# Kernel tuning notes

Hardware: AMD Instinct MI355X
Metric: run time of the kernel (lower is better)

The kernel has to match this reference:

```python
import jax, jax.numpy as jnp
import numpy as np

N, E, H, L, G, MAX_Z = 100000, 1600000, 128, 3, 1024, 1000
BN_EPS = 1e-5

def setup_inputs() -> dict:
    key = jax.random.key(0)
    ks = jax.random.split(key, 16)
    z = jax.random.randint(ks[0], (N,), 0, MAX_Z)
    edge_index = jax.random.randint(ks[1], (2, E), 0, N)
    batch = jnp.sort(jax.random.randint(ks[2], (N,), 0, G))
    s = 1.0 / np.sqrt(H)
    z_table = jax.random.normal(ks[3], (MAX_Z, H), jnp.float32)
    conv_W1 = jax.random.normal(ks[4], (L, H, H), jnp.float32) * s
    conv_b1 = jnp.zeros((L, H), jnp.float32)
    conv_W2 = jax.random.normal(ks[5], (L, H, H), jnp.float32) * s
    conv_b2 = jnp.zeros((L, H), jnp.float32)
    bn_gamma = jnp.ones((L, H), jnp.float32)
    bn_beta = jnp.zeros((L, H), jnp.float32)
    lin1_W = jax.random.normal(ks[6], (L * H, H), jnp.float32) / np.sqrt(L * H)
    lin1_b = jnp.zeros((H,), jnp.float32)
    lin2_W = jax.random.normal(ks[7], (H, 1), jnp.float32) * s
    lin2_b = jnp.zeros((1,), jnp.float32)
    return {"z": z, "edge_index": edge_index, "batch": batch,
            "z_table": z_table, "conv_W1": conv_W1, "conv_b1": conv_b1,
            "conv_W2": conv_W2, "conv_b2": conv_b2, "bn_gamma": bn_gamma,
            "bn_beta": bn_beta, "lin1_W": lin1_W, "lin1_b": lin1_b,
            "lin2_W": lin2_W, "lin2_b": lin2_b}

def _gin_layer(x, src, dst, W1, b1, W2, b2, gamma, beta):
    # GIN sum aggregation: (1+eps)*x_i + sum_{j->i} x_j  (eps=0)
    agg = x + jax.ops.segment_sum(x[src], dst, num_segments=N)
    h = jax.nn.relu(agg @ W1 + b1)
    h = jax.nn.relu(h @ W2 + b2)
    # BatchNorm1d (training-mode batch statistics over nodes)
    mu = jnp.mean(h, axis=0)
    var = jnp.mean(jnp.square(h - mu), axis=0)
    return gamma * (h - mu) * jax.lax.rsqrt(var + BN_EPS) + beta

def reference(z, edge_index, batch, z_table, conv_W1, conv_b1, conv_W2,
              conv_b2, bn_gamma, bn_beta, lin1_W, lin1_b, lin2_W, lin2_b):
    src, dst = edge_index[0], edge_index[1]
    x = z_table[z]                      # [N, H]
    xs = []
    for l in range(L):
        x = _gin_layer(x, src, dst, conv_W1[l], conv_b1[l], conv_W2[l],
                       conv_b2[l], bn_gamma[l], bn_beta[l])
        xs.append(x)
    feat = jnp.concatenate(xs, axis=1)  # [N, L*H] (jk=True)
    sums = jax.ops.segment_sum(feat, batch, num_segments=G)
    cnt = jax.ops.segment_sum(jnp.ones((N,), feat.dtype), batch, num_segments=G)
    pooled = sums / jnp.maximum(cnt, 1.0)[:, None]   # global_mean_pool [G, L*H]
    h = jax.nn.relu(pooled @ lin1_W + lin1_b)
    # dropout inactive (eval mode)
    return h @ lin2_W + lin2_b          # [G, 1]
```

## Files before the change

### kernel.cpp

```cpp
#include <hip/hip_runtime.h>

#define NN 100000
#define NE 1600000
#define HD 128
#define NL 3
#define NG 1024
#define BN_EPS 1e-5f
#define SCAN_CHUNK 1024

static inline int cdiv(int a, int b) { return (a + b - 1) / b; }

__global__ __launch_bounds__(256) void zero_counts_kernel(int* __restrict__ cnt) {
  int t = blockIdx.x * 256 + threadIdx.x;
  if (t < NN) cnt[t] = 0;
}

__global__ __launch_bounds__(256) void hist_kernel(const int* __restrict__ dstI,
    int* __restrict__ cnt) {
  int e = blockIdx.x * 256 + threadIdx.x;
  if (e < NE) atomicAdd(&cnt[dstI[e]], 1);
}

__global__ __launch_bounds__(256) void scan_block_kernel(const int* __restrict__ cnt,
    int* __restrict__ rowptr, int* __restrict__ bsums) {
  __shared__ int sh[SCAN_CHUNK];
  __shared__ int ts[256];
  int base = blockIdx.x * SCAN_CHUNK;
  for (int i = threadIdx.x; i < SCAN_CHUNK; i += 256)
    sh[i] = (base + i < NN) ? cnt[base + i] : 0;
  __syncthreads();
  int t4 = threadIdx.x * 4;
  int a0 = sh[t4], a1 = sh[t4 + 1], a2 = sh[t4 + 2], a3 = sh[t4 + 3];
  int tsum = a0 + a1 + a2 + a3;
  ts[threadIdx.x] = tsum;
  __syncthreads();
  for (int off = 1; off < 256; off <<= 1) {
    int v = ts[threadIdx.x];
    int u = (threadIdx.x >= off) ? ts[threadIdx.x - off] : 0;
    __syncthreads();
    ts[threadIdx.x] = v + u;
    __syncthreads();
  }
  int texcl = ts[threadIdx.x] - tsum;
  sh[t4] = texcl;
  sh[t4 + 1] = texcl + a0;
  sh[t4 + 2] = texcl + a0 + a1;
  sh[t4 + 3] = texcl + a0 + a1 + a2;
  __syncthreads();
  for (int i = threadIdx.x; i < SCAN_CHUNK; i += 256) {
    int g = base + i;
    if (g < NN) rowptr[g] = sh[i];
  }
  if (threadIdx.x == 255) bsums[blockIdx.x] = ts[255];
}

__global__ void scan_bsums_kernel(int* __restrict__ bsums, int nb) {
  if (threadIdx.x == 0) {
    int run = 0;
    for (int i = 0; i < nb; ++i) { int v = bsums[i]; bsums[i] = run; run += v; }
  }
}

__global__ __launch_bounds__(256) void scan_add_kernel(int* __restrict__ rowptr,
    const int* __restrict__ bsums, int* __restrict__ fill_off) {
  int t = blockIdx.x * 256 + threadIdx.x;
  if (t < NN) {
    int v = rowptr[t] + bsums[t / SCAN_CHUNK];
    rowptr[t] = v;
    fill_off[t] = v;
  }
  if (t == 0) rowptr[NN] = NE;
}

__global__ __launch_bounds__(256) void fill_kernel(const int* __restrict__ srcI,
    const int* __restrict__ dstI, const int* __restrict__ z,
    int* __restrict__ fill_off, int* __restrict__ esrc, int* __restrict__ esrcz) {
  int e = blockIdx.x * 256 + threadIdx.x;
  if (e >= NE) return;
  int s = srcI[e];
  int d = dstI[e];
  int pos = atomicAdd(&fill_off[d], 1);
  esrc[pos] = s;
  esrcz[pos] = z[s];
}

__global__ __launch_bounds__(256) void agg_kernel(const int* __restrict__ rowptr,
    const int* __restrict__ eidx, const float* __restrict__ xsrc, int xstride,
    const int* __restrict__ selfz, const float* __restrict__ ss,
    float* __restrict__ agg) {
  int n = blockIdx.x * 4 + (threadIdx.x >> 6);
  if (n >= NN) return;
  int lane = threadIdx.x & 63;
  int lo = rowptr[n], hi = rowptr[n + 1];
  int deg = hi - lo;
  int selfrow = selfz ? selfz[n] : n;
  float2 acc = *(const float2*)(xsrc + (size_t)selfrow * xstride + lane * 2);

  for (int base = 0; base < deg; base += 64) {
    int cnt = deg - base; if (cnt > 64) cnt = 64;
    int idx = (base + lane < deg) ? eidx[lo + base + lane] : 0;
    int j = 0;
    for (; j + 4 <= cnt; j += 4) {
      int s0 = __shfl(idx, j, 64);
      int s1 = __shfl(idx, j + 1, 64);
      int s2 = __shfl(idx, j + 2, 64);
      int s3 = __shfl(idx, j + 3, 64);
      float2 v0 = *(const float2*)(xsrc + (size_t)s0 * xstride + lane * 2);
      float2 v1 = *(const float2*)(xsrc + (size_t)s1 * xstride + lane * 2);
      float2 v2 = *(const float2*)(xsrc + (size_t)s2 * xstride + lane * 2);
      float2 v3 = *(const float2*)(xsrc + (size_t)s3 * xstride + lane * 2);
      acc.x += v0.x + v1.x + v2.x + v3.x;
      acc.y += v0.y + v1.y + v2.y + v3.y;
    }
    for (; j < cnt; ++j) {
      int s = __shfl(idx, j, 64);
      float2 v = *(const float2*)(xsrc + (size_t)s * xstride + lane * 2);
      acc.x += v.x; acc.y += v.y;
    }
  }

  float2 o = acc;
  if (ss) {
    float scx = ss[lane * 2], scy = ss[lane * 2 + 1];
    float shx = ss[128 + lane * 2], shy = ss[129 + lane * 2];
    float cntf = (float)(deg + 1);
    o.x = acc.x * scx + cntf * shx;
    o.y = acc.y * scy + cntf * shy;
  }
  *(float2*)(agg + (size_t)n * HD + lane * 2) = o;
}

template <int STATS>
__global__ __launch_bounds__(256) void gemm128_kernel(
    const float* __restrict__ A, const float* __restrict__ B,
    const float* __restrict__ bias, float* __restrict__ C, int cstride, int M,
    double* __restrict__ gsums) {
  __shared__ float As[32][136];
  __shared__ float Bs[32][136];
  __shared__ float csum[256];
  const int tid = threadIdx.x;
  const int row0 = blockIdx.x * 128;
  const int tr = tid >> 4;
  const int tc = tid & 15;

  if (STATS) csum[tid] = 0.f;

  float acc[8][8] = {};

  for (int kc = 0; kc < 4; ++kc) {
    __syncthreads();
    #pragma unroll
    for (int i = 0; i < 4; ++i) {
      int f = tid + i * 256;
      int row = f >> 3, kq = f & 7;
      int gr = row0 + row;
      float4 v = make_float4(0.f, 0.f, 0.f, 0.f);
      if (gr < M) v = *(const float4*)(A + (size_t)gr * HD + kc * 32 + kq * 4);
      As[kq * 4 + 0][row] = v.x; As[kq * 4 + 1][row] = v.y;
      As[kq * 4 + 2][row] = v.z; As[kq * 4 + 3][row] = v.w;
    }
    #pragma unroll
    for (int i = 0; i < 4; ++i) {
      int f = tid + i * 256;
      int k = f >> 5, c4 = (f & 31) << 2;
      *(float4*)(&Bs[k][c4]) = *(const float4*)(B + (size_t)(kc * 32 + k) * HD + c4);
    }
    __syncthreads();
    #pragma unroll
    for (int k = 0; k < 32; ++k) {
      float4 a0 = *(const float4*)(&As[k][tr * 8]);
      float4 a1 = *(const float4*)(&As[k][tr * 8 + 4]);
      float4 b0 = *(const float4*)(&Bs[k][tc * 8]);
      float4 b1 = *(const float4*)(&Bs[k][tc * 8 + 4]);
      float av[8] = {a0.x, a0.y, a0.z, a0.w, a1.x, a1.y, a1.z, a1.w};
      float bv[8] = {b0.x, b0.y, b0.z, b0.w, b1.x, b1.y, b1.z, b1.w};
      #pragma unroll
      for (int r = 0; r < 8; ++r)
        #pragma unroll
        for (int c = 0; c < 8; ++c)
          acc[r][c] += av[r] * bv[c];
    }
  }

  float4 bv0 = *(const float4*)(bias + tc * 8);
  float4 bv1 = *(const float4*)(bias + tc * 8 + 4);
  float bb[8] = {bv0.x, bv0.y, bv0.z, bv0.w, bv1.x, bv1.y, bv1.z, bv1.w};
  float ps[8] = {}, pq[8] = {};
  #pragma unroll
  for (int r = 0; r < 8; ++r) {
    int gr = row0 + tr * 8 + r;
    if (gr < M) {
      float o[8];
      #pragma unroll
      for (int c = 0; c < 8; ++c) o[c] = fmaxf(acc[r][c] + bb[c], 0.f);
      *(float4*)(C + (size_t)gr * cstride + tc * 8)     = make_float4(o[0], o[1], o[2], o[3]);
      *(float4*)(C + (size_t)gr * cstride + tc * 8 + 4) = make_float4(o[4], o[5], o[6], o[7]);
      if (STATS) {
        #pragma unroll
        for (int c = 0; c < 8; ++c) { ps[c] += o[c]; pq[c] += o[c] * o[c]; }
      }
    }
  }

  if (STATS) {
    __syncthreads();
    #pragma unroll
    for (int c = 0; c < 8; ++c) {
      atomicAdd(&csum[tc * 8 + c], ps[c]);
      atomicAdd(&csum[128 + tc * 8 + c], pq[c]);
    }
    __syncthreads();
    if (tid < 128) {
      atomicAdd(&gsums[tid], (double)csum[tid]);
      atomicAdd(&gsums[HD + tid], (double)csum[128 + tid]);
    }
  }
}

__global__ void zero_d_kernel(double* p) { p[threadIdx.x] = 0.0; }

__global__ void bn_finalize_kernel(const double* __restrict__ sums,
    const float* __restrict__ gamma, const float* __restrict__ beta,
    float* __restrict__ ss) {
  int c = threadIdx.x;
  double mu = sums[c] * (1.0 / NN);
  double var = sums[HD + c] * (1.0 / NN) - mu * mu;
  float sc = gamma[c] * (float)(1.0 / sqrt(var + (double)BN_EPS));
  ss[c] = sc;
  ss[HD + c] = beta[c] - (float)mu * sc;
}

__device__ __forceinline__ int lbound(const int* __restrict__ b, int val) {
  int lo = 0, hi = NN;
  while (lo < hi) { int m = (lo + hi) >> 1; if (b[m] < val) lo = m + 1; else hi = m; }
  return lo;
}

__global__ __launch_bounds__(384) void pool_kernel(const int* __restrict__ batch,
    const float* __restrict__ feat, const float* __restrict__ ssAll,
    float* __restrict__ pooled) {
  int g = blockIdx.x;
  int c = threadIdx.x;
  int l = c >> 7, cc = c & 127;
  float sc = ssAll[l * 256 + cc], sh = ssAll[l * 256 + 128 + cc];
  int lo = lbound(batch, g), hi = lbound(batch, g + 1);
  float s = 0.f;
  for (int r = lo; r < hi; ++r) s += feat[(size_t)r * (NL * HD) + c];
  float inv = 1.f / (float)max(hi - lo, 1);
  pooled[(size_t)g * (NL * HD) + c] = sc * (s * inv) + sh;
}

__global__ __launch_bounds__(128) void mlp_kernel(const float* __restrict__ pooled,
    const float* __restrict__ W1, const float* __restrict__ b1,
    const float* __restrict__ W2, const float* __restrict__ b2,
    float* __restrict__ out) {
  int g = blockIdx.x, c = threadIdx.x;
  const float* p = pooled + (size_t)g * (NL * HD);
  float acc = b1[c];
  #pragma unroll 4
  for (int k = 0; k < NL * HD; ++k) acc = fmaf(p[k], W1[(size_t)k * HD + c], acc);
  acc = fmaxf(acc, 0.f);
  float prod = acc * W2[c];
  #pragma unroll
  for (int off = 32; off > 0; off >>= 1) prod += __shfl_xor(prod, off, 64);
  __shared__ float part[2];
  if ((c & 63) == 0) part[c >> 6] = prod;
  __syncthreads();
  if (c == 0) out[g] = part[0] + part[1] + b2[0];
}

extern "C" void kernel_launch(void* const* d_in, const int* in_sizes, int n_in,
                              void* d_out, int out_size, void* d_ws, size_t ws_size,
                              hipStream_t stream) {
  (void)in_sizes; (void)n_in; (void)out_size; (void)ws_size;
  const int*   z     = (const int*)d_in[0];
  const int*   ei    = (const int*)d_in[1];
  const int*   batch = (const int*)d_in[2];
  const float* ztab  = (const float*)d_in[3];
  const float* W1    = (const float*)d_in[4];
  const float* b1    = (const float*)d_in[5];
  const float* W2    = (const float*)d_in[6];
  const float* b2    = (const float*)d_in[7];
  const float* gamma = (const float*)d_in[8];
  const float* beta  = (const float*)d_in[9];
  const float* l1W   = (const float*)d_in[10];
  const float* l1b   = (const float*)d_in[11];
  const float* l2W   = (const float*)d_in[12];
  const float* l2b   = (const float*)d_in[13];
  float* out = (float*)d_out;

  char* w = (char*)d_ws;
  float*  bufA   = (float*)w;  w += (size_t)NN * HD * 4;
  float*  bufB   = (float*)w;  w += (size_t)NN * HD * 4;
  float*  feat   = (float*)w;  w += (size_t)NN * (NL * HD) * 4;
  float*  pooled = (float*)w;  w += (size_t)NG * (NL * HD) * 4;
  double* sums   = (double*)w; w += 256 * 8;
  float*  ssAll  = (float*)w;  w += (size_t)NL * 256 * 4;
  int*    rowptr = (int*)w;    w += (size_t)(NN + 1) * 4;
  int*    counts = (int*)w;    w += (size_t)NN * 4;
  int*    filloff= (int*)w;    w += (size_t)NN * 4;
  int*    esrc   = (int*)w;    w += (size_t)NE * 4;
  int*    bsums  = (int*)w;    w += (size_t)cdiv(NN, SCAN_CHUNK) * 4;
  int* esrcz = (int*)bufA;

  const int* srcI = ei;
  const int* dstI = ei + NE;

  dim3 blk(256);
  const int g_nn = cdiv(NN, 256);
  const int g_ne = cdiv(NE, 256);
  const int nb_scan = cdiv(NN, SCAN_CHUNK);
  const int g_gemm = cdiv(NN, 128);

  zero_counts_kernel<<<g_nn, blk, 0, stream>>>(counts);
  hist_kernel<<<g_ne, blk, 0, stream>>>(dstI, counts);
  scan_block_kernel<<<nb_scan, blk, 0, stream>>>(counts, rowptr, bsums);
  scan_bsums_kernel<<<1, 64, 0, stream>>>(bsums, nb_scan);
  scan_add_kernel<<<g_nn, blk, 0, stream>>>(rowptr, bsums, filloff);
  fill_kernel<<<g_ne, blk, 0, stream>>>(srcI, dstI, z, filloff, esrc, esrcz);

  for (int l = 0; l < NL; ++l) {
    if (l == 0) {
      agg_kernel<<<cdiv(NN, 4), blk, 0, stream>>>(rowptr, esrcz, ztab, HD,
                                                  z, nullptr, bufB);
    } else {
      agg_kernel<<<cdiv(NN, 4), blk, 0, stream>>>(rowptr, esrc,
          feat + (l - 1) * HD, NL * HD, nullptr, ssAll + (l - 1) * 256, bufB);
    }
    gemm128_kernel<0><<<g_gemm, blk, 0, stream>>>(bufB,
        W1 + (size_t)l * HD * HD, b1 + l * HD, bufA, HD, NN, nullptr);
    zero_d_kernel<<<1, 256, 0, stream>>>(sums);
    gemm128_kernel<1><<<g_gemm, blk, 0, stream>>>(bufA,
        W2 + (size_t)l * HD * HD, b2 + l * HD, feat + l * HD, NL * HD, NN, sums);
    bn_finalize_kernel<<<1, 128, 0, stream>>>(sums, gamma + l * HD,
                                              beta + l * HD, ssAll + l * 256);
  }

  pool_kernel<<<NG, 384, 0, stream>>>(batch, feat, ssAll, pooled);
  mlp_kernel<<<NG, 128, 0, stream>>>(pooled, l1W, l1b, l2W, l2b, out);
}
```

Measured before the change: 1.141 ms.

## Replace FP32 SIMT GEMM with split-bf16 MFMA GEMM using pre-packed weight fragments

Swaps the FP32 outer-product GEMM for one built on MFMA 16x16x32 bf16 instructions. A and B are each split into hi and lo bf16 parts, and four MFMAs per tile keep accuracy close to FP32. A small pre-pass kernel packs each weight matrix into MFMA fragment layout, and the A tile is now stored row-major in LDS. This aims to cut the ALU-bound GEMM cost. In exchange it adds conversion work, uses narrower 4-byte scattered output stores, and adds extra launches for the weight split.

```diff
diff --git a/kernel.cpp b/kernel.cpp
--- a/kernel.cpp
+++ b/kernel.cpp
@@ -9,6 +9,18 @@
 #define SCAN_CHUNK 1024
 
 static inline int cdiv(int a, int b) { return (a + b - 1) / b; }
+
+typedef __attribute__((ext_vector_type(8))) short short8v;
+typedef __attribute__((ext_vector_type(4))) float f32x4;
+
+static __device__ __forceinline__ unsigned short f2bf_rne(float x) {
+  unsigned int u = __float_as_uint(x);
+  unsigned int r = (u + 0x7FFFu + ((u >> 16) & 1u)) >> 16;
+  return (unsigned short)r;
+}
+static __device__ __forceinline__ float bf2f(unsigned short s) {
+  return __uint_as_float(((unsigned int)s) << 16);
+}
 
 __global__ __launch_bounds__(256) void zero_counts_kernel(int* __restrict__ cnt) {
   int t = blockIdx.x * 256 + threadIdx.x;
@@ -130,74 +142,99 @@
   *(float2*)(agg + (size_t)n * HD + lane * 2) = o;
 }
 
+__global__ __launch_bounds__(256) void bsplit_kernel(const float* __restrict__ B,
+    short* __restrict__ bh, short* __restrict__ bl) {
+  int t = blockIdx.x * 256 + threadIdx.x;
+  if (t >= 2048) return;
+  int kc = t >> 9, ct = (t >> 6) & 7, l = t & 63;
+  int kbase = kc * 32 + (l >> 4) * 8;
+  int col = ct * 16 + (l & 15);
+  short8v H, L;
+  #pragma unroll
+  for (int j = 0; j < 8; ++j) {
+    float v = B[(size_t)(kbase + j) * HD + col];
+    unsigned short h = f2bf_rne(v);
+    float rem = v - bf2f(h);
+    H[j] = (short)h;
+    L[j] = (short)f2bf_rne(rem);
+  }
+  *(short8v*)(bh + (size_t)t * 8) = H;
+  *(short8v*)(bl + (size_t)t * 8) = L;
+}
+
 template <int STATS>
-__global__ __launch_bounds__(256) void gemm128_kernel(
-    const float* __restrict__ A, const float* __restrict__ B,
-    const float* __restrict__ bias, float* __restrict__ C, int cstride, int M,
-    double* __restrict__ gsums) {
-  __shared__ float As[32][136];
-  __shared__ float Bs[32][136];
+__global__ __launch_bounds__(256) void gemm_mfma_kernel(
+    const float* __restrict__ A, const short* __restrict__ bhS,
+    const short* __restrict__ blS, const float* __restrict__ bias,
+    float* __restrict__ C, int cstride, int M, double* __restrict__ gsums) {
+  __shared__ float As[128][36];
   __shared__ float csum[256];
   const int tid = threadIdx.x;
+  const int w = tid >> 6, l = tid & 63;
   const int row0 = blockIdx.x * 128;
-  const int tr = tid >> 4;
-  const int tc = tid & 15;
+  const int lr = l & 15, lg = l >> 4;
 
   if (STATS) csum[tid] = 0.f;
 
-  float acc[8][8] = {};
+  f32x4 c[2][8] = {};
 
   for (int kc = 0; kc < 4; ++kc) {
     __syncthreads();
     #pragma unroll
     for (int i = 0; i < 4; ++i) {
       int f = tid + i * 256;
-      int row = f >> 3, kq = f & 7;
+      int row = f >> 3, k4 = (f & 7) << 2;
       int gr = row0 + row;
       float4 v = make_float4(0.f, 0.f, 0.f, 0.f);
-      if (gr < M) v = *(const float4*)(A + (size_t)gr * HD + kc * 32 + kq * 4);
-      As[kq * 4 + 0][row] = v.x; As[kq * 4 + 1][row] = v.y;
-      As[kq * 4 + 2][row] = v.z; As[kq * 4 + 3][row] = v.w;
-    }
-    #pragma unroll
-    for (int i = 0; i < 4; ++i) {
-      int f = tid + i * 256;
-      int k = f >> 5, c4 = (f & 31) << 2;
-      *(float4*)(&Bs[k][c4]) = *(const float4*)(B + (size_t)(kc * 32 + k) * HD + c4);
-    }
-    __syncthreads();
-    #pragma unroll
-    for (int k = 0; k < 32; ++k) {
-      float4 a0 = *(const float4*)(&As[k][tr * 8]);
-      float4 a1 = *(const float4*)(&As[k][tr * 8 + 4]);
-      float4 b0 = *(const float4*)(&Bs[k][tc * 8]);
-      float4 b1 = *(const float4*)(&Bs[k][tc * 8 + 4]);
+      if (gr < M) v = *(const float4*)(A + (size_t)gr * HD + kc * 32 + k4);
+      *(float4*)(&As[row][k4]) = v;
+    }
+    __syncthreads();
+
+    short8v ahi[2], alo[2];
+    #pragma unroll
+    for (int rt = 0; rt < 2; ++rt) {
+      const float* ap = &As[w * 32 + rt * 16 + lr][lg * 8];
+      float4 a0 = *(const float4*)ap;
+      float4 a1 = *(const float4*)(ap + 4);
       float av[8] = {a0.x, a0.y, a0.z, a0.w, a1.x, a1.y, a1.z, a1.w};
-      float bv[8] = {b0.x, b0.y, b0.z, b0.w, b1.x, b1.y, b1.z, b1.w};
       #pragma unroll
-      for (int r = 0; r < 8; ++r)
-        #pragma unroll
-        for (int c = 0; c < 8; ++c)
-          acc[r][c] += av[r] * bv[c];
-    }
-  }
-
-  float4 bv0 = *(const float4*)(bias + tc * 8);
-  float4 bv1 = *(const float4*)(bias + tc * 8 + 4);
-  float bb[8] = {bv0.x, bv0.y, bv0.z, bv0.w, bv1.x, bv1.y, bv1.z, bv1.w};
+      for (int j = 0; j < 8; ++j) {
+        unsigned short h = f2bf_rne(av[j]);
+        ahi[rt][j] = (short)h;
+        alo[rt][j] = (short)f2bf_rne(av[j] - bf2f(h));
+      }
+    }
+
+    #pragma unroll
+    for (int ct = 0; ct < 8; ++ct) {
+      size_t off = ((size_t)(kc * 8 + ct) * 64 + l) * 8;
+      short8v bh = *(const short8v*)(bhS + off);
+      short8v bl = *(const short8v*)(blS + off);
+      #pragma unroll
+      for (int rt = 0; rt < 2; ++rt) {
+        c[rt][ct] = __builtin_amdgcn_mfma_f32_16x16x32_bf16(ahi[rt], bh, c[rt][ct], 0, 0, 0);
+        c[rt][ct] = __builtin_amdgcn_mfma_f32_16x16x32_bf16(alo[rt], bh, c[rt][ct], 0, 0, 0);
+        c[rt][ct] = __builtin_amdgcn_mfma_f32_16x16x32_bf16(ahi[rt], bl, c[rt][ct], 0, 0, 0);
+        c[rt][ct] = __builtin_amdgcn_mfma_f32_16x16x32_bf16(alo[rt], bl, c[rt][ct], 0, 0, 0);
+      }
+    }
+  }
+
   float ps[8] = {}, pq[8] = {};
   #pragma unroll
-  for (int r = 0; r < 8; ++r) {
-    int gr = row0 + tr * 8 + r;
-    if (gr < M) {
-      float o[8];
+  for (int ct = 0; ct < 8; ++ct) {
+    float bv = bias[ct * 16 + lr];
+    #pragma unroll
+    for (int rt = 0; rt < 2; ++rt) {
       #pragma unroll
-      for (int c = 0; c < 8; ++c) o[c] = fmaxf(acc[r][c] + bb[c], 0.f);
-      *(float4*)(C + (size_t)gr * cstride + tc * 8)     = make_float4(o[0], o[1], o[2], o[3]);
-      *(float4*)(C + (size_t)gr * cstride + tc * 8 + 4) = make_float4(o[4], o[5], o[6], o[7]);
-      if (STATS) {
-        #pragma unroll
-        for (int c = 0; c < 8; ++c) { ps[c] += o[c]; pq[c] += o[c] * o[c]; }
+      for (int i = 0; i < 4; ++i) {
+        int gr = row0 + w * 32 + rt * 16 + lg * 4 + i;
+        if (gr < M) {
+          float o = fmaxf(c[rt][ct][i] + bv, 0.f);
+          C[(size_t)gr * cstride + ct * 16 + lr] = o;
+          if (STATS) { ps[ct] += o; pq[ct] += o * o; }
+        }
       }
     }
   }
@@ -205,9 +242,9 @@
   if (STATS) {
     __syncthreads();
     #pragma unroll
-    for (int c = 0; c < 8; ++c) {
-      atomicAdd(&csum[tc * 8 + c], ps[c]);
-      atomicAdd(&csum[128 + tc * 8 + c], pq[c]);
+    for (int ct = 0; ct < 8; ++ct) {
+      atomicAdd(&csum[ct * 16 + lr], ps[ct]);
+      atomicAdd(&csum[128 + ct * 16 + lr], pq[ct]);
     }
     __syncthreads();
     if (tid < 128) {
@@ -301,6 +338,8 @@
   int*    filloff= (int*)w;    w += (size_t)NN * 4;
   int*    esrc   = (int*)w;    w += (size_t)NE * 4;
   int*    bsums  = (int*)w;    w += (size_t)cdiv(NN, SCAN_CHUNK) * 4;
+  short*  bfragH = (short*)w;  w += 2048 * 8 * 2;
+  short*  bfragL = (short*)w;  w += 2048 * 8 * 2;
   int* esrcz = (int*)bufA;
 
   const int* srcI = ei;
@@ -327,11 +366,13 @@
       agg_kernel<<<cdiv(NN, 4), blk, 0, stream>>>(rowptr, esrc,
           feat + (l - 1) * HD, NL * HD, nullptr, ssAll + (l - 1) * 256, bufB);
     }
-    gemm128_kernel<0><<<g_gemm, blk, 0, stream>>>(bufB,
-        W1 + (size_t)l * HD * HD, b1 + l * HD, bufA, HD, NN, nullptr);
+    bsplit_kernel<<<8, blk, 0, stream>>>(W1 + (size_t)l * HD * HD, bfragH, bfragL);
+    gemm_mfma_kernel<0><<<g_gemm, blk, 0, stream>>>(bufB, bfragH, bfragL,
+        b1 + l * HD, bufA, HD, NN, nullptr);
     zero_d_kernel<<<1, 256, 0, stream>>>(sums);
-    gemm128_kernel<1><<<g_gemm, blk, 0, stream>>>(bufA,
-        W2 + (size_t)l * HD * HD, b2 + l * HD, feat + l * HD, NL * HD, NN, sums);
+    bsplit_kernel<<<8, blk, 0, stream>>>(W2 + (size_t)l * HD * HD, bfragH, bfragL);
+    gemm_mfma_kernel<1><<<g_gemm, blk, 0, stream>>>(bufA, bfragH, bfragL,
+        b2 + l * HD, feat + l * HD, NL * HD, NN, sums);
     bn_finalize_kernel<<<1, 128, 0, stream>>>(sums, gamma + l * HD,
                                               beta + l * HD, ssAll + l * 256);
   }
```

After: 1.062 ms. 1.07x faster.
